# Kernel tuning notes

Hardware: AMD Instinct MI355X
Metric: run time of the kernel (lower is better)

Reference implementation:

```python
import jax, jax.numpy as jnp
import numpy as np

EMBED_DIM = 768
NUM_HEADS = 12
HEAD_DIM = EMBED_DIM // NUM_HEADS
MAX_REL = 50
B, L = 4, 1024


def setup_inputs() -> dict:
    key = jax.random.key(0)
    ks = jax.random.split(key, 8)
    query = jax.random.normal(ks[0], (B, L, EMBED_DIM), dtype=jnp.float32)
    k_in = jax.random.normal(ks[1], (B, L, EMBED_DIM), dtype=jnp.float32)
    v_in = jax.random.normal(ks[2], (B, L, EMBED_DIM), dtype=jnp.float32)
    # monotone float timestamps per batch (arange fill)
    patch_indices = jnp.arange(B * L, dtype=jnp.float32).reshape(B, L)
    std = 1.0 / np.sqrt(EMBED_DIM)
    in_proj_w = jax.random.normal(ks[3], (3 * EMBED_DIM, EMBED_DIM), dtype=jnp.float32) * std
    in_proj_b = jnp.zeros((3 * EMBED_DIM,), dtype=jnp.float32)
    out_proj_w = jax.random.normal(ks[4], (EMBED_DIM, EMBED_DIM), dtype=jnp.float32) * std
    out_proj_b = jnp.zeros((EMBED_DIM,), dtype=jnp.float32)
    rel_bias = jax.random.truncated_normal(ks[5], -2.0, 2.0, (NUM_HEADS, 2 * MAX_REL + 1), dtype=jnp.float32) * 0.1
    return {"query": query, "key": k_in, "value": v_in, "patch_indices": patch_indices,
            "in_proj_w": in_proj_w, "in_proj_b": in_proj_b,
            "out_proj_w": out_proj_w, "out_proj_b": out_proj_b, "rel_bias": rel_bias}


def _attention(query, patch_indices, in_proj_w, in_proj_b, out_proj_w, out_proj_b, rel_bias):
    Bq, Lq, D = query.shape
    H, hd, M = NUM_HEADS, HEAD_DIM, MAX_REL
    qkv = query @ in_proj_w.T + in_proj_b            # [B,L,3D]
    q, k, v = jnp.split(qkv, 3, axis=-1)
    q = q.reshape(Bq, Lq, H, hd).transpose(0, 2, 1, 3) * (hd ** -0.5)
    k = k.reshape(Bq, Lq, H, hd).transpose(0, 2, 1, 3)
    v = v.reshape(Bq, Lq, H, hd).transpose(0, 2, 1, 3)
    scores = jnp.einsum('bhld,bhmd->bhlm', q, k)     # [B,H,L,L]
    # sequence-position relative bias
    idxs = jnp.arange(Lq)
    rel_pos = jnp.clip(idxs[None, :] - idxs[:, None], -M, M) + M   # [L,L]
    scores = scores + rel_bias[:, rel_pos][None]                   # [1,H,L,L]
    # data-dependent relative-time bias
    deltas = patch_indices[:, 1:] - patch_indices[:, :-1]          # [B,L-1]
    dt = jnp.nanmedian(deltas, axis=1)
    dt = jnp.where(jnp.isfinite(dt) & (dt > 0), dt, 1.0)[:, None, None]
    rel_time = patch_indices[:, :, None] - patch_indices[:, None, :]  # [B,L,L]
    invalid = jnp.isnan(rel_time) | (rel_time < -M) | (rel_time > M)
    rel_time = jnp.where(invalid, 0.0, rel_time)
    rel_idx = (jnp.clip(jnp.round(rel_time / dt), -M, M) + M).astype(jnp.int32)  # [B,L,L]
    bias = jnp.take(rel_bias, rel_idx, axis=1)       # [H,B,L,L]
    scores = scores + jnp.moveaxis(bias, 0, 1)       # [B,H,L,L]
    probs = jax.nn.softmax(scores, axis=-1)
    out = jnp.einsum('bhlm,bhmd->bhld', probs, v)
    out = out.transpose(0, 2, 1, 3).reshape(Bq, Lq, D)
    return out @ out_proj_w.T + out_proj_b


def reference(query, key, value, patch_indices, in_proj_w, in_proj_b, out_proj_w, out_proj_b, rel_bias):
    # NOTE: the original module ignores key/value and builds qkv from query.
    return _attention(query, patch_indices, in_proj_w, in_proj_b, out_proj_w, out_proj_b, rel_bias)
```

## Files before the change

### kernel.cpp

```cpp
#include <hip/hip_runtime.h>
#include <hip/hip_bf16.h>

#define BB 4
#define LL 1024
#define DD 768
#define HH 12
#define HD 64
#define MREL 50
#define NBIAS 101
#define GK 768
#define STR 72
#define BXS 68

#define NEG_INF (-__builtin_inff())

#define QB_F   ((size_t)0)
#define KB_F   ((size_t)1572864)
#define VTB_F  ((size_t)3145728)
#define XBF_F  ((size_t)4718592)
#define WIBF_F ((size_t)6291456)
#define WOBF_F ((size_t)7176192)
#define BIDX_F ((size_t)7471104)
#define DT_F   ((size_t)9568256)

#define NQ4  (BB*LL*DD)
#define NWI4 (3*DD*DD)

typedef __attribute__((ext_vector_type(8)))  short bf16x8;
typedef __attribute__((ext_vector_type(4)))  float f32x4;
typedef __attribute__((ext_vector_type(16))) float f32x16;
typedef __attribute__((ext_vector_type(4)))  unsigned int u32x4;

__device__ __forceinline__ unsigned short f2bf(float f) {
    unsigned u = __float_as_uint(f);
    u += 0x7fffu + ((u >> 16) & 1u);
    return (unsigned short)(u >> 16);
}

__device__ __forceinline__ void gload_lds16(const void* g, void* l) {
    __builtin_amdgcn_global_load_lds(
        (const __attribute__((address_space(1))) void*)g,
        (__attribute__((address_space(3))) void*)l, 16, 0, 0);
}

__global__ __launch_bounds__(256) void prep_kernel(
    const float* __restrict__ patch, float* __restrict__ dt,
    const float* __restrict__ q, const float* __restrict__ wi, const float* __restrict__ wo,
    unsigned short* __restrict__ qd_, unsigned short* __restrict__ wid,
    unsigned short* __restrict__ wod) {
    int tid = threadIdx.x;
    if (blockIdx.x >= 4) {
        int i = ((blockIdx.x - 4) * 256 + tid) * 4;
        const float* src; unsigned short* dst; int off;
        if (i < NQ4)              { src = q;  dst = qd_; off = i; }
        else if (i < NQ4 + NWI4)  { src = wi; dst = wid; off = i - NQ4; }
        else                      { src = wo; dst = wod; off = i - NQ4 - NWI4; }
        float4 v = *(const float4*)&src[off];
        ushort4 o;
        o.x = f2bf(v.x); o.y = f2bf(v.y); o.z = f2bf(v.z); o.w = f2bf(v.w);
        *(ushort4*)&dst[off] = o;
        return;
    }
    __shared__ __align__(16) float del[1024];
    __shared__ __align__(16) unsigned long long key64[1024];
    __shared__ int nvalid;
    __shared__ float acc;
    int b = blockIdx.x;
    if (tid == 0) { nvalid = 0; acc = 0.f; }
    __syncthreads();
    int cnt = 0;
#pragma unroll
    for (int r = 0; r < 4; ++r) {
        int i = tid + r * 256;
        float v = __builtin_nanf("");
        if (i < LL - 1) {
            v = patch[b * LL + i + 1] - patch[b * LL + i];
            if (v == v) ++cnt;
        }
        del[i] = v;
        unsigned bits = (v == v) ? __float_as_uint(v) : 0x7FC00000u;
        unsigned ordk = (bits & 0x80000000u) ? ~bits : (bits | 0x80000000u);
        key64[i] = ((unsigned long long)ordk << 10) | (unsigned)i;
    }
    atomicAdd(&nvalid, cnt);
    __syncthreads();
    int i0 = tid, i1 = tid + 256, i2 = tid + 512, i3 = tid + 768;
    float v0 = del[i0], v1 = del[i1], v2 = del[i2], v3 = del[i3];
    unsigned long long k0 = key64[i0], k1 = key64[i1], k2 = key64[i2], k3 = key64[i3];
    int c0 = 0, c1 = 0, c2 = 0, c3 = 0;
#define CMPK(kx) { unsigned long long _k = (kx); \
    c0 += (_k < k0) ? 1 : 0; c1 += (_k < k1) ? 1 : 0; \
    c2 += (_k < k2) ? 1 : 0; c3 += (_k < k3) ? 1 : 0; }
    for (int j = 0; j < 1024; j += 8) {
        ulonglong2 a = *(const ulonglong2*)&key64[j];
        ulonglong2 bq = *(const ulonglong2*)&key64[j + 2];
        ulonglong2 cq = *(const ulonglong2*)&key64[j + 4];
        ulonglong2 dq = *(const ulonglong2*)&key64[j + 6];
        CMPK(a.x); CMPK(a.y); CMPK(bq.x); CMPK(bq.y);
        CMPK(cq.x); CMPK(cq.y); CMPK(dq.x); CMPK(dq.y);
    }
#undef CMPK
    int n = nvalid;
#define FIN(vr, cr) if (vr == vr) { \
    if (n & 1) { if (cr == n / 2) atomicAdd(&acc, vr); } \
    else { if (cr == n / 2 - 1 || cr == n / 2) atomicAdd(&acc, 0.5f * vr); } }
    FIN(v0, c0); FIN(v1, c1); FIN(v2, c2); FIN(v3, c3);
#undef FIN
    __syncthreads();
    if (tid == 0) {
        float m = acc;
        float res = (n > 0 && m == m && fabsf(m) != __builtin_inff() && m > 0.f) ? m : 1.0f;
        dt[b] = res;
    }
}

__global__ __launch_bounds__(256) void bidx_kernel(const float* __restrict__ patch,
                                                   const float* __restrict__ dtb,
                                                   unsigned short* __restrict__ bidx) {
    int flat = (blockIdx.x * 256 + threadIdx.x) * 8;
    int b = flat >> 20;
    int rem = flat & 1048575;
    int i = rem >> 10;
    int j0 = rem & 1023;
    float pi = patch[b * LL + i];
    float inv_dt = 1.0f / dtb[b];
    float4 pa = *(const float4*)&patch[b * LL + j0];
    float4 pb4 = *(const float4*)&patch[b * LL + j0 + 4];
    unsigned out[4];
#define MK(pj, jofs, dst, shift) { \
    int d = (j0 + jofs) - i; d = d < -MREL ? -MREL : (d > MREL ? MREL : d); \
    float rt = pi - (pj); \
    if (!(rt == rt) || rt < -(float)MREL || rt > (float)MREL) rt = 0.f; \
    float fr = fminf(fmaxf(rintf(rt * inv_dt), -(float)MREL), (float)MREL); \
    unsigned u = (unsigned)(d + MREL) | (((unsigned)((int)fr + MREL)) << 8); \
    dst |= (u << shift); }
    unsigned t;
    t = 0; MK(pa.x, 0, t, 0); MK(pa.y, 1, t, 16); out[0] = t;
    t = 0; MK(pa.z, 2, t, 0); MK(pa.w, 3, t, 16); out[1] = t;
    t = 0; MK(pb4.x, 4, t, 0); MK(pb4.y, 5, t, 16); out[2] = t;
    t = 0; MK(pb4.z, 6, t, 0); MK(pb4.w, 7, t, 16); out[3] = t;
#undef MK
    *(uint4*)&bidx[flat] = *(uint4*)&out[0];
}

#define GEMM_MAIN(SMEMN)                                                       \
    __shared__ __align__(16) unsigned short smem_g[SMEMN];                     \
    unsigned short* As = smem_g;                                               \
    unsigned short* Bs = smem_g + 8192;                                        \
    int tid = threadIdx.x;                                                     \
    int m0 = blockIdx.x << 7, n0 = blockIdx.y << 7;                            \
    int lane = tid & 63, w = tid >> 6;                                         \
    int wr = w >> 1, wc = w & 1;                                               \
    int srow = tid >> 3, scol = (tid & 7) << 3;                                \
    const unsigned short* Ag = Ab + (size_t)(m0 + srow) * GK + scol;           \
    const unsigned short* Bg = Wb + (size_t)(n0 + srow) * GK + scol;           \
    f32x4 acc[4][4];                                                           \
    _Pragma("unroll") for (int i = 0; i < 4; ++i)                              \
        _Pragma("unroll") for (int j = 0; j < 4; ++j)                          \
            acc[i][j] = (f32x4){0.f, 0.f, 0.f, 0.f};                           \
    int qd_ = lane >> 4, rl = lane & 15;                                       \
    int rA = wr * 64 + rl, rB = wc * 64 + rl;                                  \
    for (int kc = 0; kc < GK; kc += 64) {                                      \
        __syncthreads();                                                       \
        _Pragma("unroll") for (int r = 0; r < 4; ++r)                          \
            gload_lds16(Ag + (size_t)(r * 32) * GK + kc, As + tid * 8 + r * 2048); \
        _Pragma("unroll") for (int r = 0; r < 4; ++r)                          \
            gload_lds16(Bg + (size_t)(r * 32) * GK + kc, Bs + tid * 8 + r * 2048); \
        __syncthreads();                                                       \
        _Pragma("unroll") for (int ks = 0; ks < 2; ++ks) {                     \
            bf16x8 af[4], bfr[4];                                              \
            _Pragma("unroll") for (int t = 0; t < 4; ++t)                      \
                af[t] = *(const bf16x8*)&As[(rA + t * 16) * 64 + ks * 32 + qd_ * 8]; \
            _Pragma("unroll") for (int t = 0; t < 4; ++t)                      \
                bfr[t] = *(const bf16x8*)&Bs[(rB + t * 16) * 64 + ks * 32 + qd_ * 8]; \
            _Pragma("unroll") for (int i = 0; i < 4; ++i)                      \
                _Pragma("unroll") for (int j = 0; j < 4; ++j)                  \
                    acc[i][j] = __builtin_amdgcn_mfma_f32_16x16x32_bf16(       \
                        af[i], bfr[j], acc[i][j], 0, 0, 0);                    \
        }                                                                      \
    }                                                                          \
    int colL = lane & 15, rq = lane >> 4;

__global__ __launch_bounds__(256) void qkv_gemm(
    const unsigned short* __restrict__ Ab, const unsigned short* __restrict__ Wb,
    const float* __restrict__ bias,
    unsigned short* __restrict__ qb, unsigned short* __restrict__ kb,
    unsigned short* __restrict__ vtb) {
    GEMM_MAIN(17408);
    int sec = n0 / DD;
    int hh0 = (n0 - sec * DD) >> 6;
    unsigned short* Ts = smem_g;
    __syncthreads();
    if (sec == 2) {
#pragma unroll
        for (int j = 0; j < 4; ++j) {
            int col_t = wc * 64 + j * 16 + colL;
            float bn = bias[n0 + col_t];
#pragma unroll
            for (int i = 0; i < 4; ++i) {
                ushort4 o;
                o.x = f2bf(acc[i][j][0] + bn);
                o.y = f2bf(acc[i][j][1] + bn);
                o.z = f2bf(acc[i][j][2] + bn);
                o.w = f2bf(acc[i][j][3] + bn);
                *(ushort4*)&Ts[col_t * 136 + wr * 64 + i * 16 + rq * 4] = o;
            }
        }
        __syncthreads();
        int nl = tid >> 1, half = tid & 1;
        int d768 = n0 + nl - 2 * DD;
        int hh = d768 >> 6, dd = d768 & 63;
        int b = m0 >> 10, l0 = (m0 & 1023) + half * 64;
        unsigned short* dst = vtb + (((size_t)b * HH + hh) * HD + dd) * LL + l0;
#pragma unroll
        for (int k = 0; k < 8; ++k)
            *(uint4*)&dst[k * 8] = *(const uint4*)&Ts[nl * 136 + half * 64 + k * 8];
    } else {
        float scale = (sec == 0) ? 0.18033688011112042f : 1.0f;
#pragma unroll
        for (int j = 0; j < 4; ++j) {
            int col_t = wc * 64 + j * 16 + colL;
            float bn = bias[n0 + col_t];
#pragma unroll
            for (int i = 0; i < 4; ++i) {
                int row_t = wr * 64 + i * 16 + rq * 4;
#pragma unroll
                for (int r = 0; r < 4; ++r)
                    Ts[(row_t + r) * 136 + col_t] = f2bf((acc[i][j][r] + bn) * scale);
            }
        }
        __syncthreads();
        int ml = tid >> 1, half = tid & 1;
        int b = (m0 + ml) >> 10, l = (m0 + ml) & 1023;
        unsigned short* dst = (sec == 0 ? qb : kb)
                              + (((size_t)b * HH + hh0 + half) * LL + l) * HD;
#pragma unroll
        for (int k = 0; k < 8; ++k)
            *(uint4*)&dst[k * 8] = *(const uint4*)&Ts[ml * 136 + half * 64 + k * 8];
    }
}

__global__ __launch_bounds__(256) void out_gemm(
    const unsigned short* __restrict__ Ab, const unsigned short* __restrict__ Wb,
    const float* __restrict__ bias, float* __restrict__ C) {
    GEMM_MAIN(16384);
#pragma unroll
    for (int j = 0; j < 4; ++j) {
        int n = n0 + wc * 64 + j * 16 + colL;
        float bn = bias[n];
#pragma unroll
        for (int i = 0; i < 4; ++i) {
            int rowb = m0 + wr * 64 + i * 16 + rq * 4;
#pragma unroll
            for (int r = 0; r < 4; ++r)
                C[(size_t)(rowb + r) * DD + n] = acc[i][j][r] + bn;
        }
    }
}

__global__ __launch_bounds__(256) void attn_kernel(
    const unsigned short* __restrict__ QB, const unsigned short* __restrict__ KB,
    const unsigned short* __restrict__ VTB, const unsigned short* __restrict__ BIDX,
    const float* __restrict__ relb, unsigned short* __restrict__ aout) {
    __shared__ __align__(16) unsigned short smem[2 * 64 * STR + 64 * BXS];
    __shared__ float sb[NBIAS];
    __shared__ float psum_s[128];
    __shared__ float linv_s[64];
    unsigned short* Ks  = smem;
    unsigned short* Vt  = smem + 64 * STR;
    unsigned short* Bxs = smem + 2 * 64 * STR;
    float* fcomb = (float*)smem;

    int tid = threadIdx.x;
    int w = tid >> 6, lane = tid & 63, li = lane & 31, qd = lane >> 5;
    int jt = w & 1, it = w >> 1;
    int bh = blockIdx.x, b = bh / HH, h = bh - b * HH;
    int q0 = blockIdx.y << 6;
    if (tid < NBIAS) sb[tid] = relb[h * NBIAS + tid] * 1.44269504088896340736f;
    int i_loc = it * 32 + li;
    int i_abs = q0 + i_loc;
    bf16x8 kq[4];
    const unsigned short* qrow = QB + ((size_t)bh * LL + i_abs) * HD + qd * 8;
#pragma unroll
    for (int ks = 0; ks < 4; ++ks) kq[ks] = *(const bf16x8*)(qrow + ks * 16);
    float l_run = 0.f;
    f32x16 O0, O1;
#pragma unroll
    for (int r = 0; r < 16; ++r) { O0[r] = 0.f; O1[r] = 0.f; }
    int srow = tid >> 3, sc = (tid & 7) << 3;
    const unsigned short* kgb = KB + (size_t)bh * LL * HD;
    const unsigned short* vgb = VTB + (size_t)bh * HD * LL;
    const unsigned short* bxg = BIDX + ((size_t)b << 20) + (size_t)q0 * 1024;
    bf16x8 kvr[2], vvr[2], bxr[2];
#pragma unroll
    for (int rep = 0; rep < 2; ++rep) {
        int r = srow + rep * 32;
        kvr[rep] = *(const bf16x8*)(kgb + (size_t)r * HD + sc);
        vvr[rep] = *(const bf16x8*)(vgb + (size_t)r * LL + sc);
        bxr[rep] = *(const bf16x8*)(bxg + (size_t)r * 1024 + sc);
    }
    __syncthreads();
    float sb0 = sb[0], sb100 = sb[100];
    for (int kt = 0; kt < 16; ++kt) {
        __syncthreads();
#pragma unroll
        for (int rep = 0; rep < 2; ++rep) {
            int r = srow + rep * 32;
            *(bf16x8*)&Ks[r * STR + sc] = kvr[rep];
            *(bf16x8*)&Vt[r * STR + sc] = vvr[rep];
            *(bf16x8*)&Bxs[r * BXS + sc] = bxr[rep];
        }
        if (kt + 1 < 16) {
#pragma unroll
            for (int rep = 0; rep < 2; ++rep) {
                int r = srow + rep * 32;
                kvr[rep] = *(const bf16x8*)(kgb + (size_t)((kt + 1) * 64 + r) * HD + sc);
                vvr[rep] = *(const bf16x8*)(vgb + (size_t)r * LL + (kt + 1) * 64 + sc);
                bxr[rep] = *(const bf16x8*)(bxg + (size_t)r * 1024 + (kt + 1) * 64 + sc);
            }
        }
        __syncthreads();
        f32x16 st;
#pragma unroll
        for (int r = 0; r < 16; ++r) st[r] = 0.f;
#pragma unroll
        for (int ks = 0; ks < 4; ++ks) {
            bf16x8 ak = *(const bf16x8*)&Ks[(jt * 32 + li) * STR + ks * 16 + qd * 8];
            st = __builtin_amdgcn_mfma_f32_32x32x16_bf16(ak, kq[ks], st, 0, 0, 0);
        }
        int delta = (kt << 6) + (jt << 5) - q0 - (it << 5);
        if (delta >= 81 || delta <= -81) {
            float db = (delta >= 81) ? sb100 : sb0;
#pragma unroll
            for (int g4 = 0; g4 < 4; ++g4) {
                ushort4 bi = *(const ushort4*)&Bxs[i_loc * BXS + jt * 32 + g4 * 8 + qd * 4];
#pragma unroll
                for (int q = 0; q < 4; ++q) {
                    int r = g4 * 4 + q;
                    unsigned u = (q == 0) ? bi.x : (q == 1) ? bi.y : (q == 2) ? bi.z : bi.w;
                    st[r] = st[r] + db + sb[u >> 8];
                }
            }
        } else {
#pragma unroll
            for (int g4 = 0; g4 < 4; ++g4) {
                ushort4 bi = *(const ushort4*)&Bxs[i_loc * BXS + jt * 32 + g4 * 8 + qd * 4];
#pragma unroll
                for (int q = 0; q < 4; ++q) {
                    int r = g4 * 4 + q;
                    unsigned u = (q == 0) ? bi.x : (q == 1) ? bi.y : (q == 2) ? bi.z : bi.w;
                    st[r] = st[r] + sb[u & 0xffu] + sb[u >> 8];
                }
            }
        }
        float rs = 0.f;
        unsigned W[8];
#pragma unroll
        for (int pr = 0; pr < 8; ++pr) {
            float p0 = __builtin_amdgcn_exp2f(st[2 * pr]);
            float p1 = __builtin_amdgcn_exp2f(st[2 * pr + 1]);
            rs += p0 + p1;
            unsigned wpk;
            asm("v_cvt_pk_bf16_f32 %0, %1, %2" : "=v"(wpk) : "v"(p0), "v"(p1));
            W[pr] = wpk;
        }
        rs += __shfl_xor(rs, 32);
        l_run += rs;
        auto s02 = __builtin_amdgcn_permlane32_swap(W[0], W[2], false, false);
        auto s13 = __builtin_amdgcn_permlane32_swap(W[1], W[3], false, false);
        auto s46 = __builtin_amdgcn_permlane32_swap(W[4], W[6], false, false);
        auto s57 = __builtin_amdgcn_permlane32_swap(W[5], W[7], false, false);
        u32x4 a0w = {(unsigned)s02[0], (unsigned)s13[0], (unsigned)s02[1], (unsigned)s13[1]};
        u32x4 a1w = {(unsigned)s46[0], (unsigned)s57[0], (unsigned)s46[1], (unsigned)s57[1]};
        bf16x8 ap0 = __builtin_bit_cast(bf16x8, a0w);
        bf16x8 ap1 = __builtin_bit_cast(bf16x8, a1w);
        {
            bf16x8 bv;
            bv = *(const bf16x8*)&Vt[(li) * STR + jt * 32 + qd * 8];
            O0 = __builtin_amdgcn_mfma_f32_32x32x16_bf16(ap0, bv, O0, 0, 0, 0);
            bv = *(const bf16x8*)&Vt[(li) * STR + jt * 32 + 16 + qd * 8];
            O0 = __builtin_amdgcn_mfma_f32_32x32x16_bf16(ap1, bv, O0, 0, 0, 0);
            bv = *(const bf16x8*)&Vt[(32 + li) * STR + jt * 32 + qd * 8];
            O1 = __builtin_amdgcn_mfma_f32_32x32x16_bf16(ap0, bv, O1, 0, 0, 0);
            bv = *(const bf16x8*)&Vt[(32 + li) * STR + jt * 32 + 16 + qd * 8];
            O1 = __builtin_amdgcn_mfma_f32_32x32x16_bf16(ap1, bv, O1, 0, 0, 0);
        }
    }
    if (qd == 0) psum_s[jt * 64 + i_loc] = l_run;
    __syncthreads();
    if (jt == 0 && qd == 0)
        linv_s[i_loc] = 1.0f / (psum_s[i_loc] + psum_s[64 + i_loc]);
    if (jt == 1) {
        int ibase = it * 32;
#pragma unroll
        for (int r = 0; r < 16; ++r) {
            int irow = (r & 3) + ((r >> 2) << 3) + (qd << 2);
            fcomb[(ibase + irow) * 64 + li] = O0[r];
            fcomb[(ibase + irow) * 64 + 32 + li] = O1[r];
        }
    }
    __syncthreads();
    if (jt == 0) {
        int ibase = it * 32;
#pragma unroll
        for (int r = 0; r < 16; ++r) {
            int irow = (r & 3) + ((r >> 2) << 3) + (qd << 2);
            float inv = linv_s[ibase + irow];
            float v0 = (O0[r] + fcomb[(ibase + irow) * 64 + li]) * inv;
            float v1 = (O1[r] + fcomb[(ibase + irow) * 64 + 32 + li]) * inv;
            size_t rowoff = (size_t)(b * LL + q0 + ibase + irow) * DD + h * HD;
            aout[rowoff + li] = f2bf(v0);
            aout[rowoff + 32 + li] = f2bf(v1);
        }
    }
}

extern "C" void kernel_launch(void* const* d_in, const int* in_sizes, int n_in,
                              void* d_out, int out_size, void* d_ws, size_t ws_size,
                              hipStream_t stream) {
    const float* query    = (const float*)d_in[0];
    const float* patch    = (const float*)d_in[3];
    const float* in_w     = (const float*)d_in[4];
    const float* in_b     = (const float*)d_in[5];
    const float* out_w    = (const float*)d_in[6];
    const float* out_b    = (const float*)d_in[7];
    const float* rel_bias = (const float*)d_in[8];
    float* ws  = (float*)d_ws;
    float* out = (float*)d_out;

    unsigned short* qb   = (unsigned short*)(ws + QB_F);
    unsigned short* kb   = (unsigned short*)(ws + KB_F);
    unsigned short* vtb  = (unsigned short*)(ws + VTB_F);
    unsigned short* xbf  = (unsigned short*)(ws + XBF_F);
    unsigned short* wibf = (unsigned short*)(ws + WIBF_F);
    unsigned short* wobf = (unsigned short*)(ws + WOBF_F);
    unsigned short* bidx = (unsigned short*)(ws + BIDX_F);

    prep_kernel<<<5380, 256, 0, stream>>>(patch, ws + DT_F, query, in_w, out_w,
                                          xbf, wibf, wobf);
    bidx_kernel<<<2048, 256, 0, stream>>>(patch, ws + DT_F, bidx);
    qkv_gemm<<<dim3(32, 18), 256, 0, stream>>>(xbf, wibf, in_b, qb, kb, vtb);
    attn_kernel<<<dim3(BB * HH, LL / 64), 256, 0, stream>>>(
        qb, kb, vtb, bidx, rel_bias, xbf);
    out_gemm<<<dim3(32, 6), 256, 0, stream>>>(xbf, wobf, out_b, out);
}
```

Measured before the change: 217.1 us.

## Double-buffer GEMM LDS staging, shrink M tile to 64, swizzle LDS columns

Both projection GEMMs now stage A/B tiles into two alternating LDS buffers, so the next k-chunk load is issued before computing the current one and one barrier per iteration is removed. The M tile is halved from 128 to 64 rows, doubling the grid (64x18 and 64x6 blocks) so more blocks are resident on the GPU, and each wave now covers 64x32 outputs instead of 64x64. An XOR swizzle on LDS column chunks aims to reduce bank conflicts on the bf16x8 fragment reads. Costs are more LDS per block, less reuse of each B tile, and reworked epilogue indexing for the Q/K/V transposed writes.

```diff
diff --git a/kernel.cpp b/kernel.cpp
--- a/kernel.cpp
+++ b/kernel.cpp
@@ -143,41 +143,50 @@
     *(uint4*)&bidx[flat] = *(uint4*)&out[0];
 }
 
-#define GEMM_MAIN(SMEMN)                                                       \
-    __shared__ __align__(16) unsigned short smem_g[SMEMN];                     \
-    unsigned short* As = smem_g;                                               \
-    unsigned short* Bs = smem_g + 8192;                                        \
+#define STAGE_DB(boff, kc)                                                     \
+    { _Pragma("unroll") for (int r = 0; r < 2; ++r)                            \
+          gload_lds16(Ag + (size_t)(r * 32) * GK + (kc),                       \
+                      smem_g + (boff) + r * 2048 + tid * 8);                   \
+      _Pragma("unroll") for (int r = 0; r < 4; ++r)                            \
+          gload_lds16(Bg + (size_t)(r * 32) * GK + (kc),                       \
+                      smem_g + (boff) + 4096 + r * 2048 + tid * 8); }
+
+#define GEMM_DB_MAIN()                                                         \
+    __shared__ __align__(16) unsigned short smem_g[24576];                     \
     int tid = threadIdx.x;                                                     \
-    int m0 = blockIdx.x << 7, n0 = blockIdx.y << 7;                            \
+    int m0 = blockIdx.x << 6, n0 = blockIdx.y << 7;                            \
     int lane = tid & 63, w = tid >> 6;                                         \
-    int wr = w >> 1, wc = w & 1;                                               \
-    int srow = tid >> 3, scol = (tid & 7) << 3;                                \
+    int srow = tid >> 3;                                                       \
+    int scol = (((tid & 7) ^ (srow & 7)) << 3);   \
     const unsigned short* Ag = Ab + (size_t)(m0 + srow) * GK + scol;           \
     const unsigned short* Bg = Wb + (size_t)(n0 + srow) * GK + scol;           \
-    f32x4 acc[4][4];                                                           \
+    f32x4 acc[4][2];                                                           \
     _Pragma("unroll") for (int i = 0; i < 4; ++i)                              \
-        _Pragma("unroll") for (int j = 0; j < 4; ++j)                          \
+        _Pragma("unroll") for (int j = 0; j < 2; ++j)                          \
             acc[i][j] = (f32x4){0.f, 0.f, 0.f, 0.f};                           \
-    int qd_ = lane >> 4, rl = lane & 15;                                       \
-    int rA = wr * 64 + rl, rB = wc * 64 + rl;                                  \
-    for (int kc = 0; kc < GK; kc += 64) {                                      \
-        __syncthreads();                                                       \
-        _Pragma("unroll") for (int r = 0; r < 4; ++r)                          \
-            gload_lds16(Ag + (size_t)(r * 32) * GK + kc, As + tid * 8 + r * 2048); \
-        _Pragma("unroll") for (int r = 0; r < 4; ++r)                          \
-            gload_lds16(Bg + (size_t)(r * 32) * GK + kc, Bs + tid * 8 + r * 2048); \
-        __syncthreads();                                                       \
+    int qd_ = lane >> 4, rl = lane & 15, xA = rl & 7;                          \
+    int rB = w * 32 + rl;                                                      \
+    STAGE_DB(0, 0);                                                            \
+    int cur = 0;                                                               \
+    for (int t = 0; t < GK / 64; ++t) {                                        \
+        __syncthreads();    \
+        if (t + 1 < GK / 64) STAGE_DB((cur ^ 1) * 12288, (t + 1) * 64);        \
+        int bo = cur * 12288;                                                  \
+        const unsigned short* Abl = smem_g + bo;                               \
+        const unsigned short* Bbl = smem_g + bo + 4096;                        \
         _Pragma("unroll") for (int ks = 0; ks < 2; ++ks) {                     \
-            bf16x8 af[4], bfr[4];                                              \
-            _Pragma("unroll") for (int t = 0; t < 4; ++t)                      \
-                af[t] = *(const bf16x8*)&As[(rA + t * 16) * 64 + ks * 32 + qd_ * 8]; \
-            _Pragma("unroll") for (int t = 0; t < 4; ++t)                      \
-                bfr[t] = *(const bf16x8*)&Bs[(rB + t * 16) * 64 + ks * 32 + qd_ * 8]; \
+            int cb = ((ks * 4 + qd_) ^ xA) << 3;        \
+            bf16x8 af[4], bfr[2];                                              \
             _Pragma("unroll") for (int i = 0; i < 4; ++i)                      \
-                _Pragma("unroll") for (int j = 0; j < 4; ++j)                  \
+                af[i] = *(const bf16x8*)&Abl[(rl + i * 16) * 64 + cb];         \
+            _Pragma("unroll") for (int j = 0; j < 2; ++j)                      \
+                bfr[j] = *(const bf16x8*)&Bbl[(rB + j * 16) * 64 + cb];        \
+            _Pragma("unroll") for (int i = 0; i < 4; ++i)                      \
+                _Pragma("unroll") for (int j = 0; j < 2; ++j)                  \
                     acc[i][j] = __builtin_amdgcn_mfma_f32_16x16x32_bf16(       \
                         af[i], bfr[j], acc[i][j], 0, 0, 0);                    \
         }                                                                      \
+        cur ^= 1;                                                              \
     }                                                                          \
     int colL = lane & 15, rq = lane >> 4;
 
@@ -186,15 +195,15 @@
     const float* __restrict__ bias,
     unsigned short* __restrict__ qb, unsigned short* __restrict__ kb,
     unsigned short* __restrict__ vtb) {
-    GEMM_MAIN(17408);
+    GEMM_DB_MAIN();
     int sec = n0 / DD;
     int hh0 = (n0 - sec * DD) >> 6;
     unsigned short* Ts = smem_g;
     __syncthreads();
     if (sec == 2) {
 #pragma unroll
-        for (int j = 0; j < 4; ++j) {
-            int col_t = wc * 64 + j * 16 + colL;
+        for (int j = 0; j < 2; ++j) {
+            int col_t = w * 32 + j * 16 + colL;
             float bn = bias[n0 + col_t];
 #pragma unroll
             for (int i = 0; i < 4; ++i) {
@@ -203,54 +212,55 @@
                 o.y = f2bf(acc[i][j][1] + bn);
                 o.z = f2bf(acc[i][j][2] + bn);
                 o.w = f2bf(acc[i][j][3] + bn);
-                *(ushort4*)&Ts[col_t * 136 + wr * 64 + i * 16 + rq * 4] = o;
+                *(ushort4*)&Ts[col_t * 72 + i * 16 + rq * 4] = o;
             }
         }
         __syncthreads();
         int nl = tid >> 1, half = tid & 1;
         int d768 = n0 + nl - 2 * DD;
         int hh = d768 >> 6, dd = d768 & 63;
-        int b = m0 >> 10, l0 = (m0 & 1023) + half * 64;
+        int b = m0 >> 10, l0 = (m0 & 1023) + half * 32;
         unsigned short* dst = vtb + (((size_t)b * HH + hh) * HD + dd) * LL + l0;
 #pragma unroll
-        for (int k = 0; k < 8; ++k)
-            *(uint4*)&dst[k * 8] = *(const uint4*)&Ts[nl * 136 + half * 64 + k * 8];
+        for (int k = 0; k < 4; ++k)
+            *(uint4*)&dst[k * 8] = *(const uint4*)&Ts[nl * 72 + half * 32 + k * 8];
     } else {
         float scale = (sec == 0) ? 0.18033688011112042f : 1.0f;
 #pragma unroll
-        for (int j = 0; j < 4; ++j) {
-            int col_t = wc * 64 + j * 16 + colL;
+        for (int j = 0; j < 2; ++j) {
+            int col_t = w * 32 + j * 16 + colL;
             float bn = bias[n0 + col_t];
 #pragma unroll
             for (int i = 0; i < 4; ++i) {
-                int row_t = wr * 64 + i * 16 + rq * 4;
+                int row_t = i * 16 + rq * 4;
 #pragma unroll
                 for (int r = 0; r < 4; ++r)
                     Ts[(row_t + r) * 136 + col_t] = f2bf((acc[i][j][r] + bn) * scale);
             }
         }
         __syncthreads();
-        int ml = tid >> 1, half = tid & 1;
+        int ml = tid >> 2, q4 = tid & 3;
         int b = (m0 + ml) >> 10, l = (m0 + ml) & 1023;
         unsigned short* dst = (sec == 0 ? qb : kb)
-                              + (((size_t)b * HH + hh0 + half) * LL + l) * HD;
-#pragma unroll
-        for (int k = 0; k < 8; ++k)
-            *(uint4*)&dst[k * 8] = *(const uint4*)&Ts[ml * 136 + half * 64 + k * 8];
+                              + (((size_t)b * HH + hh0 + (q4 >> 1)) * LL + l) * HD
+                              + (q4 & 1) * 32;
+#pragma unroll
+        for (int k = 0; k < 4; ++k)
+            *(uint4*)&dst[k * 8] = *(const uint4*)&Ts[ml * 136 + q4 * 32 + k * 8];
     }
 }
 
 __global__ __launch_bounds__(256) void out_gemm(
     const unsigned short* __restrict__ Ab, const unsigned short* __restrict__ Wb,
     const float* __restrict__ bias, float* __restrict__ C) {
-    GEMM_MAIN(16384);
-#pragma unroll
-    for (int j = 0; j < 4; ++j) {
-        int n = n0 + wc * 64 + j * 16 + colL;
+    GEMM_DB_MAIN();
+#pragma unroll
+    for (int j = 0; j < 2; ++j) {
+        int n = n0 + w * 32 + j * 16 + colL;
         float bn = bias[n];
 #pragma unroll
         for (int i = 0; i < 4; ++i) {
-            int rowb = m0 + wr * 64 + i * 16 + rq * 4;
+            int rowb = m0 + i * 16 + rq * 4;
 #pragma unroll
             for (int r = 0; r < 4; ++r)
                 C[(size_t)(rowb + r) * DD + n] = acc[i][j][r] + bn;
@@ -439,8 +449,8 @@
     prep_kernel<<<5380, 256, 0, stream>>>(patch, ws + DT_F, query, in_w, out_w,
                                           xbf, wibf, wobf);
     bidx_kernel<<<2048, 256, 0, stream>>>(patch, ws + DT_F, bidx);
-    qkv_gemm<<<dim3(32, 18), 256, 0, stream>>>(xbf, wibf, in_b, qb, kb, vtb);
+    qkv_gemm<<<dim3(64, 18), 256, 0, stream>>>(xbf, wibf, in_b, qb, kb, vtb);
     attn_kernel<<<dim3(BB * HH, LL / 64), 256, 0, stream>>>(
         qb, kb, vtb, bidx, rel_bias, xbf);
-    out_gemm<<<dim3(32, 6), 256, 0, stream>>>(xbf, wobf, out_b, out);
-}
+    out_gemm<<<dim3(64, 6), 256, 0, stream>>>(xbf, wobf, out_b, out);
+}
```

After: 191.4 us (median of 2 runs). -11.8%, faster.
